# Performance work log

Measured on AMD Instinct MI355X. Metric: run time of the kernel, lower is better.

Reference implementation:

```python
import jax, jax.numpy as jnp
import numpy as np
from jax import lax

N = 100000   # total nodes in batched graph
E = 3200000  # total edges
B = 32       # graphs in batch
L = 1000     # text sequence length (required by mx3 kernel=108)
D = 128      # emb_dim
H = 3        # heads of gcn1
OD = 128     # output_dim


def setup_inputs() -> dict:
    key = jax.random.key(0)
    ks = jax.random.split(key, 32)
    def p(i, shape, s=0.05):
        return jax.random.normal(ks[i], shape, jnp.float32) * s
    return {
        "node_feat": p(0, (N, D), 1.0),
        "src": jax.random.randint(ks[1], (E,), 0, N),
        "dst": jax.random.randint(ks[2], (E,), 0, N),
        "graph_ids": jnp.sort(jax.random.randint(ks[3], (N,), 0, B)),
        "pad_dmap": p(4, (B, 1, L, D), 1.0),
        # GATConv 1: in=D, out=D, heads=3
        "W1": p(5, (D, H * D)), "al1": p(6, (H, D)), "ar1": p(7, (H, D)), "b1": p(8, (H * D,)),
        # GATConv 2: in=3D, out=3D, heads=1
        "W2": p(9, (H * D, H * D)), "al2": p(10, (1, H * D)), "ar2": p(11, (1, H * D)), "b2": p(12, (H * D,)),
        "fc_g1_w": p(13, (H * D, OD)), "fc_g1_b": p(14, (OD,)),
        # Conv1d weights in torch OIH layout
        "conv1_w": p(15, (128, D, 3)), "conv1_b": p(16, (128,)),
        "conv2_w": p(17, (128, 128, 3)), "conv2_b": p(18, (128,)),
        "conv3_w": p(19, (128, 128, 3)), "conv3_b": p(20, (128,)),
        "tf_w": p(21, (128, OD)), "tf_b": p(22, (OD,)),
        "w1": jnp.array([0.5], jnp.float32),
        "fc1_w": p(23, (OD, 512)), "fc1_b": p(24, (512,)),
        "fc2_w": p(25, (512, 256)), "fc2_b": p(26, (256,)),
        "out_w": p(27, (256, 2)), "out_b": p(28, (2,)),
    }


def _gat(feat, src, dst, W, al, ar, b, heads, od):
    """DGL GATConv (feat_drop=attn_drop=0, negative_slope=0.2, bias)."""
    n = feat.shape[0]
    h = (feat @ W).reshape(n, heads, od)                 # [N,H,od]
    el = jnp.einsum('nhd,hd->nh', h, al)                 # [N,H]
    er = jnp.einsum('nhd,hd->nh', h, ar)
    e = jax.nn.leaky_relu(el[src] + er[dst], 0.2)        # [E,H] per-edge score
    m = jax.ops.segment_max(e, dst, num_segments=n)
    m = jnp.where(jnp.isfinite(m), m, 0.0)               # isolated nodes -> 0
    a = jnp.exp(e - m[dst])
    s = jax.ops.segment_sum(a, dst, num_segments=n)
    alpha = a / s[dst]                                   # edge softmax over in-neighborhood
    rst = jax.ops.segment_sum(alpha[:, :, None] * h[src], dst, num_segments=n)
    return rst + b.reshape(1, heads, od)


def _conv1d(x, w, b):
    y = lax.conv_general_dilated(x, w, (1,), 'VALID', dimension_numbers=('NCH', 'OIH', 'NCH'))
    return y + b[None, :, None]


def _maxpool1d(x, k, s):
    return lax.reduce_window(x, -jnp.inf, lax.max, (1, 1, k), (1, 1, s), 'VALID')


def reference(node_feat, src, dst, graph_ids, pad_dmap,
              W1, al1, ar1, b1, W2, al2, ar2, b2,
              fc_g1_w, fc_g1_b, conv1_w, conv1_b, conv2_w, conv2_b,
              conv3_w, conv3_b, tf_w, tf_b, w1,
              fc1_w, fc1_b, fc2_w, fc2_b, out_w, out_b):
    relu = jax.nn.relu
    # graph branch
    g = relu(_gat(node_feat, src, dst, W1, al1, ar1, b1, H, D)).reshape(-1, H * D)
    g = relu(_gat(g, src, dst, W2, al2, ar2, b2, 1, H * D)).reshape(-1, H * D)
    gpool = jax.ops.segment_max(g, graph_ids, num_segments=B)   # graph max pooling [B,384]
    g1 = relu(gpool @ fc_g1_w + fc_g1_b)
    # text CNN branch
    x = pad_dmap[:, 0].transpose(0, 2, 1)                       # [B, D, L]
    f = _maxpool1d(_conv1d(x, conv1_w, conv1_b), 3, 3)
    f = _maxpool1d(_conv1d(f, conv2_w, conv2_b), 3, 3)
    f = _maxpool1d(_conv1d(f, conv3_w, conv3_b), 108, 1)[:, :, 0]  # [B,128]
    seq1 = relu(f @ tf_w + tf_b)
    # weighted fusion + MLP head (dropout is identity in eval)
    wv = jax.nn.sigmoid(w1)
    gc = (1.0 - wv) * g1 + wv * seq1
    gc = relu(gc @ fc1_w + fc1_b)
    gc = relu(gc @ fc2_w + fc2_b)
    o = relu(gc @ out_w + out_b)
    return jax.nn.softmax(o, axis=1)
```

## Files before the change

### kernel.cpp

```cpp
#include <hip/hip_runtime.h>
#include <math.h>

constexpr int NN = 100000;
constexpr int EE = 3200000;
constexpr int BB = 32;
constexpr int LSEQ = 1000;
constexpr int DD = 128;
constexpr int NH = 3;
constexpr int HD = 384;
constexpr int NB1 = (NN + 255) / 256;
constexpr int NMT = (NN + 127) / 128;

typedef __attribute__((ext_vector_type(8))) short bf16v8;
typedef __attribute__((ext_vector_type(4))) float f32x4;

static __device__ __forceinline__ float lrelu(float x) { return x > 0.f ? x : 0.2f * x; }
static __device__ __forceinline__ float bf2f(unsigned short u) {
  return __uint_as_float(((unsigned)u) << 16);
}
static __device__ __forceinline__ unsigned short f2bf(float f) {
  unsigned x = __float_as_uint(f);
  return (unsigned short)((x + 0x7fffu + ((x >> 16) & 1u)) >> 16);
}

constexpr int PB_NF   = (NN * DD / 4) / 256;
constexpr int PB_PAD  = (BB * LSEQ * 128 / 4) / 256;
constexpr int PB_DEG  = NB1;
constexpr int PB_EL2  = (2 * NN + 255) / 256;
constexpr int PB_GP   = (BB * HD + 255) / 256;
constexpr int PB_TW1  = (128 * 384 + 255) / 256;
constexpr int PB_TW2  = (384 * 384 + 255) / 256;
constexpr int PB_TC   = (128 * 384 + 255) / 256;
constexpr int PREP_BLOCKS = PB_NF + PB_PAD + PB_DEG + PB_EL2 + PB_GP + PB_TW1 + PB_TW2 + 3 * PB_TC;

__global__ void prep_misc(const float* __restrict__ nf, unsigned short* __restrict__ nfbf,
                          const float* __restrict__ pad, unsigned short* __restrict__ padbf,
                          int* __restrict__ deg, float* __restrict__ el2z,
                          unsigned* __restrict__ gpool,
                          const float* __restrict__ W1, unsigned short* __restrict__ Wt1,
                          const float* __restrict__ W2, unsigned short* __restrict__ Wt2,
                          const float* __restrict__ c1w, unsigned short* __restrict__ Wc1,
                          const float* __restrict__ c2w, unsigned short* __restrict__ Wc2,
                          const float* __restrict__ c3w, unsigned short* __restrict__ Wc3) {
  int bx = blockIdx.x, tid = threadIdx.x;
  if (bx < PB_NF) {
    int i = bx * 256 + tid;
    float4 v = ((const float4*)nf)[i];
    ushort4 o;
    o.x = f2bf(v.x); o.y = f2bf(v.y); o.z = f2bf(v.z); o.w = f2bf(v.w);
    ((ushort4*)nfbf)[i] = o;
    return;
  }
  bx -= PB_NF;
  if (bx < PB_PAD) {
    int i = bx * 256 + tid;
    float4 v = ((const float4*)pad)[i];
    ushort4 o;
    o.x = f2bf(v.x); o.y = f2bf(v.y); o.z = f2bf(v.z); o.w = f2bf(v.w);
    ((ushort4*)padbf)[i] = o;
    return;
  }
  bx -= PB_PAD;
  if (bx < PB_DEG) {
    int i = bx * 256 + tid;
    if (i < NN) deg[i] = 0;
    return;
  }
  bx -= PB_DEG;
  if (bx < PB_EL2) {
    int i = bx * 256 + tid;
    if (i < 2 * NN) el2z[i] = 0.f;
    return;
  }
  bx -= PB_EL2;
  if (bx < PB_GP) {
    int i = bx * 256 + tid;
    if (i < BB * HD) gpool[i] = 0u;
    return;
  }
  bx -= PB_GP;
  if (bx < PB_TW1) {
    int id = bx * 256 + tid;
    if (id < 384 * 128) { int n = id / 128, k = id % 128; Wt1[id] = f2bf(W1[(size_t)k * 384 + n]); }
    return;
  }
  bx -= PB_TW1;
  if (bx < PB_TW2) {
    int id = bx * 256 + tid;
    if (id < 384 * 384) { int n = id / 384, k = id % 384; Wt2[id] = f2bf(W2[(size_t)k * 384 + n]); }
    return;
  }
  bx -= PB_TW2;
  const float* cw = (bx < PB_TC) ? c1w : (bx < 2 * PB_TC) ? c2w : c3w;
  unsigned short* co = (bx < PB_TC) ? Wc1 : (bx < 2 * PB_TC) ? Wc2 : Wc3;
  int id = (bx % PB_TC) * 256 + tid;
  if (id < 128 * 384) {
    int o = id / 384, rem = id % 384;
    int t = rem / 128, i = rem % 128;
    co[id] = f2bf(cw[(size_t)o * 384 + i * 3 + t]);
  }
}

__global__ void hist_k(const int* __restrict__ dst, int* __restrict__ deg,
                       int* __restrict__ rank) {
  int i = blockIdx.x * 256 + threadIdx.x;
  if (i >= EE / 4) return;
  int4 d = ((const int4*)dst)[i];
  int4 r;
  r.x = atomicAdd(&deg[d.x], 1);
  r.y = atomicAdd(&deg[d.y], 1);
  r.z = atomicAdd(&deg[d.z], 1);
  r.w = atomicAdd(&deg[d.w], 1);
  ((int4*)rank)[i] = r;
}

__global__ void scan1_k(const int* __restrict__ deg, int* __restrict__ excl,
                        int* __restrict__ bsum) {
  __shared__ int tmp[256];
  int tid = threadIdx.x;
  int i = blockIdx.x * 256 + tid;
  int v = (i < NN) ? deg[i] : 0;
  tmp[tid] = v;
  __syncthreads();
  for (int off = 1; off < 256; off <<= 1) {
    int t = (tid >= off) ? tmp[tid - off] : 0;
    __syncthreads();
    tmp[tid] += t;
    __syncthreads();
  }
  if (i < NN) excl[i] = tmp[tid] - v;
  if (tid == 255) bsum[blockIdx.x] = tmp[255];
}

__global__ void scan2p(int* __restrict__ bsum) {
  __shared__ int tmp[512];
  int tid = threadIdx.x;
  int v = (tid < NB1) ? bsum[tid] : 0;
  tmp[tid] = v;
  __syncthreads();
  for (int off = 1; off < 512; off <<= 1) {
    int t = (tid >= off) ? tmp[tid - off] : 0;
    __syncthreads();
    tmp[tid] += t;
    __syncthreads();
  }
  if (tid < NB1) bsum[tid] = tmp[tid] - v;
}

__global__ void scan3_k(const int* __restrict__ excl, const int* __restrict__ bsum,
                        int* __restrict__ offs) {
  int i = blockIdx.x * 256 + threadIdx.x;
  if (i < NN) offs[i] = excl[i] + bsum[blockIdx.x];
}

__global__ void scatter_k(const int* __restrict__ src, const int* __restrict__ dst,
                          const int* __restrict__ rank, const int* __restrict__ offs,
                          int* __restrict__ srcs) {
  int i = blockIdx.x * 256 + threadIdx.x;
  if (i >= EE / 4) return;
  int4 s = ((const int4*)src)[i];
  int4 d = ((const int4*)dst)[i];
  int4 r = ((const int4*)rank)[i];
  srcs[offs[d.x] + r.x] = s.x;
  srcs[offs[d.y] + r.y] = s.y;
  srcs[offs[d.z] + r.z] = s.z;
  srcs[offs[d.w] + r.w] = s.w;
}

template <int NKB, bool BRES>
__global__ __launch_bounds__(512) void gemm_nres(const unsigned short* __restrict__ A,
                                                 const unsigned short* __restrict__ Bt,
                                                 unsigned short* __restrict__ C,
                                                 const float* __restrict__ al,
                                                 const float* __restrict__ ar,
                                                 float* __restrict__ el,
                                                 float* __restrict__ er,
                                                 int M, int Nc, int nmt, int mpb) {
  static_assert(!BRES || NKB <= 2, "resident B needs K<=128");
  constexpr int KTOT = NKB * 64;
  __shared__ unsigned short As[2][8192];
  __shared__ unsigned short Bs[16384];
  __shared__ float elbuf[128][4];
  __shared__ float erbuf[128][4];
  int tid = threadIdx.x;
  int lane = tid & 63;
  int wave = tid >> 6;
  int wm = wave >> 2, wn = wave & 3;
  int tile_n = blockIdx.x * 128;
  int rloc = lane >> 3;
  int cs = (lane & 7) ^ rloc;
  const unsigned short* Bb = Bt + (size_t)tile_n * KTOT;

  int c0 = tile_n + wn * 32 + (lane & 15);
  float alv0 = al[c0], alv1 = al[c0 + 16];
  float arv0 = ar[c0], arv1 = ar[c0 + 16];

  int mt0 = blockIdx.y * mpb;
  if (mt0 >= nmt) return;
  int mt1 = min(mt0 + mpb, nmt);

  auto stage_a = [&](int mt, int kb, int buf) {
    const unsigned short* Ab = A + (size_t)mt * 128 * KTOT;
    int mr = M - 1 - mt * 128;
#pragma unroll
    for (int q = 0; q < 2; ++q) {
      int t = wave * 2 + q, r = t * 8 + rloc;
      int ra = r > mr ? mr : r;
      __builtin_amdgcn_global_load_lds(
          (const __attribute__((address_space(1))) void*)(Ab + (size_t)ra * KTOT + kb * 64 + cs * 8),
          (__attribute__((address_space(3))) void*)(&As[buf][t * 512]), 16, 0, 0);
    }
  };
  auto stage_b = [&](int kb, int buf) {
#pragma unroll
    for (int q = 0; q < 2; ++q) {
      int t = wave * 2 + q, r = t * 8 + rloc;
      __builtin_amdgcn_global_load_lds(
          (const __attribute__((address_space(1))) void*)(Bb + (size_t)r * KTOT + kb * 64 + cs * 8),
          (__attribute__((address_space(3))) void*)(&Bs[buf * 8192 + t * 512]), 16, 0, 0);
    }
  };

  f32x4 acc[4][2];
#pragma unroll
  for (int i = 0; i < 4; ++i)
#pragma unroll
    for (int j = 0; j < 2; ++j) acc[i][j] = (f32x4){0.f, 0.f, 0.f, 0.f};

  if constexpr (BRES) {
#pragma unroll
    for (int kb = 0; kb < NKB; ++kb) stage_b(kb, kb);
  } else {
    stage_b(0, 0);
  }
  stage_a(mt0, 0, 0);
  __syncthreads();

  int nsteps = (mt1 - mt0) * NKB;
  for (int i = 0; i < nsteps; ++i) {
    int mt = mt0 + i / NKB;
    int kb = i % NKB;
    int cb = i & 1;
    if (i + 1 < nsteps) {
      int ni = i + 1;
      stage_a(mt0 + ni / NKB, ni % NKB, ni & 1);
      if constexpr (!BRES) stage_b(ni % NKB, ni & 1);
    }
    const unsigned short* Ablk = &As[cb][0];
    const unsigned short* Bblk = BRES ? (Bs + kb * 8192) : (Bs + cb * 8192);
#pragma unroll
    for (int ks = 0; ks < 2; ++ks) {
      int q = ks * 4 + (lane >> 4);
      bf16v8 af[4], bfr[2];
#pragma unroll
      for (int ii = 0; ii < 4; ++ii) {
        int r = wm * 64 + ii * 16 + (lane & 15);
        af[ii] = *(const bf16v8*)&Ablk[r * 64 + ((q ^ (r & 7)) * 8)];
      }
#pragma unroll
      for (int j = 0; j < 2; ++j) {
        int r = wn * 32 + j * 16 + (lane & 15);
        bfr[j] = *(const bf16v8*)&Bblk[r * 64 + ((q ^ (r & 7)) * 8)];
      }
#pragma unroll
      for (int ii = 0; ii < 4; ++ii)
#pragma unroll
        for (int j = 0; j < 2; ++j)
          acc[ii][j] = __builtin_amdgcn_mfma_f32_16x16x32_bf16(af[ii], bfr[j], acc[ii][j], 0, 0, 0);
    }
    if (kb == NKB - 1) {
#pragma unroll
      for (int ii = 0; ii < 4; ++ii) {
        int row0 = mt * 128 + wm * 64 + ii * 16 + (lane >> 4) * 4;
#pragma unroll
        for (int j = 0; j < 2; ++j) {
          int col = tile_n + wn * 32 + j * 16 + (lane & 15);
#pragma unroll
          for (int p = 0; p < 4; ++p) {
            int row = row0 + p;
            if (row < M) C[(size_t)row * Nc + col] = f2bf(acc[ii][j][p]);
          }
        }
      }
#pragma unroll
      for (int ii = 0; ii < 4; ++ii) {
#pragma unroll
        for (int p = 0; p < 4; ++p) {
          float pe = acc[ii][0][p] * alv0 + acc[ii][1][p] * alv1;
          float pr = acc[ii][0][p] * arv0 + acc[ii][1][p] * arv1;
#pragma unroll
          for (int off = 1; off < 16; off <<= 1) {
            pe += __shfl_xor(pe, off);
            pr += __shfl_xor(pr, off);
          }
          if ((lane & 15) == 0) {
            int rl = wm * 64 + ii * 16 + (lane >> 4) * 4 + p;
            elbuf[rl][wn] = pe;
            erbuf[rl][wn] = pr;
          }
        }
      }
      __syncthreads();
      if (tid < 128) {
        int row = mt * 128 + tid;
        if (row < M) {
          float ev = elbuf[tid][0] + elbuf[tid][1] + elbuf[tid][2] + elbuf[tid][3];
          float rv = erbuf[tid][0] + erbuf[tid][1] + erbuf[tid][2] + erbuf[tid][3];
          if constexpr (BRES) {
            el[row * 4 + blockIdx.x] = ev;
            er[row * 4 + blockIdx.x] = rv;
          } else {
            atomicAdd(&el[row], ev);
            atomicAdd(&er[row], rv);
          }
        }
      }
#pragma unroll
      for (int ii = 0; ii < 4; ++ii)
#pragma unroll
        for (int j = 0; j < 2; ++j) acc[ii][j] = (f32x4){0.f, 0.f, 0.f, 0.f};
    }
    __syncthreads();
  }
}

__global__ __launch_bounds__(256) void gemm_mfma(const unsigned short* __restrict__ A,
                                                 int lda,
                                                 const unsigned short* __restrict__ Bt,
                                                 unsigned short* __restrict__ C,
                                                 int M, int K, int Nc,
                                                 const float* __restrict__ bias,
                                                 long aBatch, long cBatch) {
  __shared__ unsigned short As[128 * 64];
  __shared__ unsigned short Bs[128 * 64];
  int lane = threadIdx.x & 63;
  int wave = threadIdx.x >> 6;
  int wm = wave >> 1, wn = wave & 1;
  int tile_m = blockIdx.y * 128;
  int tile_n = blockIdx.x * 128;
  int maxRa = M - 1 - tile_m;
  f32x4 acc[4][4];
#pragma unroll
  for (int i = 0; i < 4; ++i)
#pragma unroll
    for (int j = 0; j < 4; ++j) acc[i][j] = (f32x4){0.f, 0.f, 0.f, 0.f};

  const unsigned short* Ab = A + (size_t)blockIdx.z * aBatch + (size_t)tile_m * lda;
  unsigned short* Cb = C + (size_t)blockIdx.z * cBatch;
  const unsigned short* Bb = Bt + (size_t)tile_n * K;
  int rloc = (lane >> 3);
  int cs = (lane & 7) ^ rloc;

  for (int k0 = 0; k0 < K; k0 += 64) {
#pragma unroll
    for (int q = 0; q < 4; ++q) {
      int t = wave * 4 + q;
      int r = t * 8 + rloc;
      int ra = r > maxRa ? maxRa : r;
      __builtin_amdgcn_global_load_lds(
          (const __attribute__((address_space(1))) void*)(Ab + (size_t)ra * lda + k0 + cs * 8),
          (__attribute__((address_space(3))) void*)(As + t * 512), 16, 0, 0);
      __builtin_amdgcn_global_load_lds(
          (const __attribute__((address_space(1))) void*)(Bb + (size_t)r * K + k0 + cs * 8),
          (__attribute__((address_space(3))) void*)(Bs + t * 512), 16, 0, 0);
    }
    __syncthreads();
#pragma unroll
    for (int ks = 0; ks < 2; ++ks) {
      int q = ks * 4 + (lane >> 4);
      bf16v8 af[4], bfr[4];
#pragma unroll
      for (int i = 0; i < 4; ++i) {
        int r = wm * 64 + i * 16 + (lane & 15);
        af[i] = *(const bf16v8*)&As[r * 64 + ((q ^ (r & 7)) * 8)];
      }
#pragma unroll
      for (int j = 0; j < 4; ++j) {
        int r = wn * 64 + j * 16 + (lane & 15);
        bfr[j] = *(const bf16v8*)&Bs[r * 64 + ((q ^ (r & 7)) * 8)];
      }
#pragma unroll
      for (int i = 0; i < 4; ++i)
#pragma unroll
        for (int j = 0; j < 4; ++j)
          acc[i][j] = __builtin_amdgcn_mfma_f32_16x16x32_bf16(af[i], bfr[j], acc[i][j], 0, 0, 0);
    }
    __syncthreads();
  }
#pragma unroll
  for (int i = 0; i < 4; ++i) {
    int row0 = tile_m + wm * 64 + i * 16 + (lane >> 4) * 4;
#pragma unroll
    for (int j = 0; j < 4; ++j) {
      int col = tile_n + wn * 64 + j * 16 + (lane & 15);
      float bv = bias ? bias[col] : 0.f;
#pragma unroll
      for (int p = 0; p < 4; ++p) {
        int row = row0 + p;
        if (row < M) Cb[(size_t)row * Nc + col] = f2bf(acc[i][j][p] + bv);
      }
    }
  }
}

template <int H>
static __device__ __forceinline__ void agg_body3(const float4 t,
                                                 const unsigned short* __restrict__ hfeat,
                                                 int lane, float acc[6]) {
  int s2 = __float_as_int(t.w);
  const unsigned short* hrow = hfeat + (size_t)s2 * HD;
  uint2 va = *(const uint2*)(hrow + lane * 4);
  unsigned vb = *(const unsigned*)(hrow + 256 + lane * 2);
  float wa = (H == 3) ? ((lane < 32) ? t.x : t.y) : t.x;
  float wc = (H == 3) ? t.z : t.x;
  acc[0] += wa * bf2f((unsigned short)(va.x & 0xffffu));
  acc[1] += wa * bf2f((unsigned short)(va.x >> 16));
  acc[2] += wa * bf2f((unsigned short)(va.y & 0xffffu));
  acc[3] += wa * bf2f((unsigned short)(va.y >> 16));
  acc[4] += wc * bf2f((unsigned short)(vb & 0xffffu));
  acc[5] += wc * bf2f((unsigned short)(vb >> 16));
}

template <int H>
static __device__ __forceinline__ void load_sc(const float* __restrict__ el,
                                               int s, const float erd[H], float sc[H]) {
  if constexpr (H == 3) {
    float4 e = ((const float4*)el)[s];
    sc[0] = lrelu(e.x + erd[0]);
    sc[1] = lrelu(e.y + erd[1]);
    sc[2] = lrelu(e.z + erd[2]);
  } else {
    sc[0] = lrelu(el[s] + erd[0]);
  }
}

template <int H>
__global__ __launch_bounds__(256) void agg_csr3(const int* __restrict__ offs,
                                                const int* __restrict__ deg,
                                                const int* __restrict__ srcs,
                                                const float* __restrict__ el,
                                                const float* __restrict__ er,
                                                const unsigned short* __restrict__ hfeat,
                                                const float* __restrict__ bias,
                                                unsigned short* __restrict__ outg) {
  __shared__ float wb[4][64][4];
  int wave = threadIdx.x >> 6, lane = threadIdx.x & 63;
  int d = blockIdx.x * 4 + wave;
  int o0 = offs[d], dg = deg[d];
  float erd[H];
  if constexpr (H == 3) {
    float4 e = ((const float4*)er)[d];
    erd[0] = e.x; erd[1] = e.y; erd[2] = e.z;
  } else {
    erd[0] = er[d];
  }
  float acc[6] = {0.f, 0.f, 0.f, 0.f, 0.f, 0.f};
  float wsum[H];
#pragma unroll
  for (int h = 0; h < H; ++h) wsum[h] = 0.f;

  if (dg <= 64) {
    bool has = lane < dg;
    int s = has ? srcs[o0 + lane] : 0;
    float sc[H], mh[H];
    load_sc<H>(el, s, erd, sc);
#pragma unroll
    for (int h = 0; h < H; ++h) {
      if (!has) sc[h] = -1e30f;
      mh[h] = sc[h];
#pragma unroll
      for (int off = 1; off < 64; off <<= 1) mh[h] = fmaxf(mh[h], __shfl_xor(mh[h], off));
    }
    float w0 = 0.f, w1 = 0.f, w2 = 0.f;
    if (has) {
      w0 = __expf(sc[0] - mh[0]);
      if constexpr (H == 3) {
        w1 = __expf(sc[1] - mh[1]);
        w2 = __expf(sc[2] - mh[2]);
      }
    }
    wsum[0] = w0;
    if constexpr (H == 3) { wsum[1] = w1; wsum[2] = w2; }
    *(float4*)&wb[wave][lane][0] = make_float4(w0, w1, w2, __int_as_float(s));
#pragma unroll 16
    for (int j = 0; j < dg; ++j) {
      float4 t = *(const float4*)&wb[wave][j][0];
      agg_body3<H>(t, hfeat, lane, acc);
    }
  } else {
    float mh[H];
#pragma unroll
    for (int h = 0; h < H; ++h) mh[h] = -1e30f;
    for (int e = lane; e < dg; e += 64) {
      int s = srcs[o0 + e];
      float sc[H];
      load_sc<H>(el, s, erd, sc);
#pragma unroll
      for (int h = 0; h < H; ++h) mh[h] = fmaxf(mh[h], sc[h]);
    }
#pragma unroll
    for (int h = 0; h < H; ++h) {
#pragma unroll
      for (int off = 1; off < 64; off <<= 1) mh[h] = fmaxf(mh[h], __shfl_xor(mh[h], off));
    }
    int nch = (dg + 63) >> 6;
    for (int ch = 0; ch < nch; ++ch) {
      int e = ch * 64 + lane;
      bool has = e < dg;
      int s = has ? srcs[o0 + e] : 0;
      float sc[H];
      load_sc<H>(el, s, erd, sc);
      float w0 = 0.f, w1 = 0.f, w2 = 0.f;
      if (has) {
        w0 = __expf(sc[0] - mh[0]);
        if constexpr (H == 3) {
          w1 = __expf(sc[1] - mh[1]);
          w2 = __expf(sc[2] - mh[2]);
        }
      }
      wsum[0] += w0;
      if constexpr (H == 3) { wsum[1] += w1; wsum[2] += w2; }
      *(float4*)&wb[wave][lane][0] = make_float4(w0, w1, w2, __int_as_float(s));
      int cnt = min(64, dg - ch * 64);
#pragma unroll 16
      for (int j = 0; j < cnt; ++j) {
        float4 t = *(const float4*)&wb[wave][j][0];
        agg_body3<H>(t, hfeat, lane, acc);
      }
    }
  }
#pragma unroll
  for (int h = 0; h < H; ++h) {
#pragma unroll
    for (int off = 1; off < 64; off <<= 1) wsum[h] += __shfl_xor(wsum[h], off);
  }
  float swA = (H == 3) ? ((lane < 32) ? wsum[0] : wsum[1]) : wsum[0];
  float swC = (H == 3) ? wsum[H - 1] : wsum[0];
  float invA = (dg > 0) ? 1.f / swA : 0.f;
  float invC = (dg > 0) ? 1.f / swC : 0.f;
  unsigned short* orow = outg + (size_t)d * HD;
  int cA = lane * 4, cB = 256 + lane * 2;
  float r0 = fmaxf(acc[0] * invA + bias[cA + 0], 0.f);
  float r1 = fmaxf(acc[1] * invA + bias[cA + 1], 0.f);
  float r2 = fmaxf(acc[2] * invA + bias[cA + 2], 0.f);
  float r3 = fmaxf(acc[3] * invA + bias[cA + 3], 0.f);
  float r4 = fmaxf(acc[4] * invC + bias[cB + 0], 0.f);
  float r5 = fmaxf(acc[5] * invC + bias[cB + 1], 0.f);
  uint2 pa;
  pa.x = (unsigned)f2bf(r0) | ((unsigned)f2bf(r1) << 16);
  pa.y = (unsigned)f2bf(r2) | ((unsigned)f2bf(r3) << 16);
  *(uint2*)(orow + cA) = pa;
  *(unsigned*)(orow + cB) = (unsigned)f2bf(r4) | ((unsigned)f2bf(r5) << 16);
}

__global__ void graph_pool(const unsigned short* __restrict__ g, const int* __restrict__ gid,
                           unsigned* __restrict__ gp) {
  int c = threadIdx.x;
  int n0 = blockIdx.x * 64;
  int nend = min(n0 + 64, NN);
  int cur = gid[n0];
  float mx = 0.f;
  for (int n = n0; n < nend; ++n) {
    int gg = gid[n];
    if (gg != cur) {
      atomicMax(&gp[cur * HD + c], __float_as_uint(mx));
      cur = gg; mx = 0.f;
    }
    mx = fmaxf(mx, bf2f(g[(size_t)n * HD + c]));
  }
  atomicMax(&gp[cur * HD + c], __float_as_uint(mx));
}

__global__ void maxpool_nhc(const unsigned short* __restrict__ in, unsigned short* __restrict__ out,
                            int Lin, int Lout, int total) {
  int idx = blockIdx.x * 256 + threadIdx.x;
  if (idx >= total) return;
  int c = idx & 127;
  int j = (idx >> 7) % Lout;
  int b = idx / (128 * Lout);
  const unsigned short* p = in + ((size_t)b * Lin + j * 3) * 128 + c;
  float m = bf2f(p[0]);
  m = fmaxf(m, bf2f(p[128]));
  m = fmaxf(m, bf2f(p[256]));
  out[idx] = f2bf(m);
}

__global__ void gpool_c3(const unsigned short* __restrict__ in, float* __restrict__ fvec) {
  int idx = blockIdx.x * 256 + threadIdx.x;
  if (idx >= BB * 128) return;
  int c = idx & 127, b = idx >> 7;
  const unsigned short* p = in + (size_t)b * 108 * 128 + c;
  float m = bf2f(p[0]);
  for (int t = 1; t < 108; ++t) m = fmaxf(m, bf2f(p[t * 128]));
  fvec[idx] = m;
}

__global__ __launch_bounds__(256) void head_all(const unsigned* __restrict__ gpool,
                                                const float* __restrict__ fvec,
                                                const float* __restrict__ fcgw,
                                                const float* __restrict__ fcgb,
                                                const float* __restrict__ tfw,
                                                const float* __restrict__ tfb,
                                                const float* __restrict__ w1s,
                                                const float* __restrict__ fc1w,
                                                const float* __restrict__ fc1b,
                                                const float* __restrict__ fc2w,
                                                const float* __restrict__ fc2b,
                                                const float* __restrict__ outw,
                                                const float* __restrict__ outb,
                                                float* __restrict__ out) {
  __shared__ float gl[HD];
  __shared__ float gcv[128];
  __shared__ float gc1[512];
  __shared__ float gc2[256];
  int b = blockIdx.x, tid = threadIdx.x;
  for (int c = tid; c < HD; c += 256) gl[c] = __uint_as_float(gpool[b * HD + c]);
  __syncthreads();
  float wv = 1.f / (1.f + __expf(-w1s[0]));
  if (tid < 128) {
    float a = fcgb[tid];
    for (int k = 0; k < HD; ++k) a += gl[k] * fcgw[(size_t)k * 128 + tid];
    float g1 = fmaxf(a, 0.f);
    float s = tfb[tid];
    const float* fv = fvec + b * 128;
    for (int k = 0; k < 128; ++k) s += fv[k] * tfw[(size_t)k * 128 + tid];
    float s1 = fmaxf(s, 0.f);
    gcv[tid] = (1.f - wv) * g1 + wv * s1;
  }
  __syncthreads();
#pragma unroll
  for (int q = 0; q < 2; ++q) {
    int j = tid + q * 256;
    float a = fc1b[j];
    for (int k = 0; k < 128; ++k) a += gcv[k] * fc1w[(size_t)k * 512 + j];
    gc1[j] = fmaxf(a, 0.f);
  }
  __syncthreads();
  {
    float a = fc2b[tid];
    for (int k = 0; k < 512; ++k) a += gc1[k] * fc2w[(size_t)k * 256 + tid];
    gc2[tid] = fmaxf(a, 0.f);
  }
  __syncthreads();
  if (tid < 64) {
    float p0 = 0.f, p1 = 0.f;
#pragma unroll
    for (int q = 0; q < 4; ++q) {
      float v = gc2[tid + q * 64];
      p0 += v * outw[(tid + q * 64) * 2 + 0];
      p1 += v * outw[(tid + q * 64) * 2 + 1];
    }
#pragma unroll
    for (int off = 32; off; off >>= 1) {
      p0 += __shfl_down(p0, off);
      p1 += __shfl_down(p1, off);
    }
    if (tid == 0) {
      float o0 = fmaxf(p0 + outb[0], 0.f), o1 = fmaxf(p1 + outb[1], 0.f);
      float mm = fmaxf(o0, o1);
      float e0 = __expf(o0 - mm), e1 = __expf(o1 - mm);
      float inv = 1.f / (e0 + e1);
      out[b * 2 + 0] = e0 * inv;
      out[b * 2 + 1] = e1 * inv;
    }
  }
}

extern "C" void kernel_launch(void* const* d_in, const int* in_sizes, int n_in,
                              void* d_out, int out_size, void* d_ws, size_t ws_size,
                              hipStream_t stream) {
  const float* node_feat = (const float*)d_in[0];
  const int*   src  = (const int*)d_in[1];
  const int*   dst  = (const int*)d_in[2];
  const int*   gids = (const int*)d_in[3];
  const float* pad  = (const float*)d_in[4];
  const float* W1   = (const float*)d_in[5];
  const float* al1  = (const float*)d_in[6];
  const float* ar1  = (const float*)d_in[7];
  const float* b1   = (const float*)d_in[8];
  const float* W2   = (const float*)d_in[9];
  const float* al2  = (const float*)d_in[10];
  const float* ar2  = (const float*)d_in[11];
  const float* b2   = (const float*)d_in[12];
  const float* fcgw = (const float*)d_in[13];
  const float* fcgb = (const float*)d_in[14];
  const float* c1w  = (const float*)d_in[15];
  const float* c1b  = (const float*)d_in[16];
  const float* c2w  = (const float*)d_in[17];
  const float* c2b  = (const float*)d_in[18];
  const float* c3w  = (const float*)d_in[19];
  const float* c3b  = (const float*)d_in[20];
  const float* tfw  = (const float*)d_in[21];
  const float* tfb  = (const float*)d_in[22];
  const float* w1s  = (const float*)d_in[23];
  const float* fc1w = (const float*)d_in[24];
  const float* fc1b = (const float*)d_in[25];
  const float* fc2w = (const float*)d_in[26];
  const float* fc2b = (const float*)d_in[27];
  const float* outw = (const float*)d_in[28];
  const float* outb = (const float*)d_in[29];
  float* out = (float*)d_out;
  char* base = (char*)d_ws;

  constexpr size_t SZ_BIG = (size_t)NN * HD * 2;
  unsigned short* hA = (unsigned short*)(base + 0);
  unsigned short* gB = (unsigned short*)(base + SZ_BIG);
  unsigned short* nfbf = gB;
  size_t o = 2 * SZ_BIG;
  unsigned short* Wt1 = (unsigned short*)(base + o); o += 384 * 128 * 2;
  unsigned short* Wt2 = (unsigned short*)(base + o); o += 384 * 384 * 2;
  unsigned short* Wc1 = (unsigned short*)(base + o); o += 128 * 384 * 2;
  unsigned short* Wc2 = (unsigned short*)(base + o); o += 128 * 384 * 2;
  unsigned short* Wc3 = (unsigned short*)(base + o); o += 128 * 384 * 2;
  int* deg    = (int*)(base + o); o += (size_t)NN * 4;
  int* offs   = (int*)(base + o); o += (size_t)NN * 4;
  int* excl   = (int*)(base + o); o += (size_t)NN * 4;
  int* bsum   = (int*)(base + o); o += 2048;
  int* srcs   = (int*)(base + o); o += (size_t)EE * 4;
  int* rank   = (int*)(base + o); o += (size_t)EE * 4;
  float* el1  = (float*)(base + o); o += (size_t)NN * 4 * 4;
  float* er1  = (float*)(base + o); o += (size_t)NN * 4 * 4;
  float* el2  = (float*)(base + o); o += (size_t)NN * 4;
  float* er2  = (float*)(base + o); o += (size_t)NN * 4;
  unsigned* gpool = (unsigned*)(base + o); o += (size_t)BB * HD * 4;
  float* fvec = (float*)(base + o); o += BB * 128 * 4;

  unsigned short* padbf = (unsigned short*)base;
  unsigned short* c1bf  = padbf + (size_t)BB * LSEQ * 128;
  unsigned short* p1bf  = c1bf + (size_t)BB * 998 * 128;
  unsigned short* c2bf  = p1bf + (size_t)BB * 332 * 128;
  unsigned short* p2bf  = c2bf + (size_t)BB * 330 * 128;
  unsigned short* c3bf  = p2bf + (size_t)BB * 110 * 128;

  prep_misc<<<PREP_BLOCKS, 256, 0, stream>>>(node_feat, nfbf, pad, padbf, deg, el2, gpool,
                                             W1, Wt1, W2, Wt2, c1w, Wc1, c2w, Wc2, c3w, Wc3);

  gemm_mfma<<<dim3(1, 8, BB), 256, 0, stream>>>(padbf, 128, Wc1, c1bf, 998, 384, 128, c1b,
                                                (long)LSEQ * 128, (long)998 * 128);
  maxpool_nhc<<<(BB * 332 * 128 + 255) / 256, 256, 0, stream>>>(c1bf, p1bf, 998, 332, BB * 332 * 128);
  gemm_mfma<<<dim3(1, 3, BB), 256, 0, stream>>>(p1bf, 128, Wc2, c2bf, 330, 384, 128, c2b,
                                                (long)332 * 128, (long)330 * 128);
  maxpool_nhc<<<(BB * 110 * 128 + 255) / 256, 256, 0, stream>>>(c2bf, p2bf, 330, 110, BB * 110 * 128);
  gemm_mfma<<<dim3(1, 1, BB), 256, 0, stream>>>(p2bf, 128, Wc3, c3bf, 108, 384, 128, c3b,
                                                (long)110 * 128, (long)108 * 128);
  gpool_c3<<<(BB * 128 + 255) / 256, 256, 0, stream>>>(c3bf, fvec);

  hist_k<<<EE / 1024, 256, 0, stream>>>(dst, deg, rank);
  scan1_k<<<NB1, 256, 0, stream>>>(deg, excl, bsum);
  scan2p<<<1, 512, 0, stream>>>(bsum);
  scan3_k<<<NB1, 256, 0, stream>>>(excl, bsum, offs);
  scatter_k<<<EE / 1024, 256, 0, stream>>>(src, dst, rank, offs, srcs);

  gemm_nres<2, true><<<dim3(3, (NMT + 9) / 10), 512, 0, stream>>>(
      nfbf, Wt1, hA, al1, ar1, el1, er1, NN, HD, NMT, 10);
  agg_csr3<3><<<NN / 4, 256, 0, stream>>>(offs, deg, srcs, el1, er1, hA, b1, gB);

  gemm_nres<6, false><<<dim3(3, (NMT + 9) / 10), 512, 0, stream>>>(
      gB, Wt2, hA, al2, ar2, el2, er2, NN, HD, NMT, 10);
  agg_csr3<1><<<NN / 4, 256, 0, stream>>>(offs, deg, srcs, el2, er2, hA, b2, gB);

  graph_pool<<<(NN + 63) / 64, 384, 0, stream>>>(gB, gids, gpool);
  head_all<<<BB, 256, 0, stream>>>(gpool, fvec, fcgw, fcgb, tfw, tfb, w1s,
                                   fc1w, fc1b, fc2w, fc2b, outw, outb, out);
}
```

Before: 1.264 ms.

## Fuse graph max-pooling into second GAT aggregation and text pool into head

The second aggregation kernel now does graph max-pooling itself with per-element atomicMax into the pooled buffer, instead of writing node features and running a separate pool kernel. Each lane now handles six contiguous channels, loaded with a uint3 access. The text-branch global max-pool kernel is folded into the head kernel. The aim is to avoid the full node-feature write and re-read plus two launches, but it adds millions of contended atomics on a few addresses.

```diff
diff --git a/kernel.cpp b/kernel.cpp
--- a/kernel.cpp
+++ b/kernel.cpp
@@ -406,19 +406,25 @@
 template <int H>
 static __device__ __forceinline__ void agg_body3(const float4 t,
                                                  const unsigned short* __restrict__ hfeat,
-                                                 int lane, float acc[6]) {
+                                                 int cbase, float acc[6]) {
   int s2 = __float_as_int(t.w);
-  const unsigned short* hrow = hfeat + (size_t)s2 * HD;
-  uint2 va = *(const uint2*)(hrow + lane * 4);
-  unsigned vb = *(const unsigned*)(hrow + 256 + lane * 2);
-  float wa = (H == 3) ? ((lane < 32) ? t.x : t.y) : t.x;
-  float wc = (H == 3) ? t.z : t.x;
-  acc[0] += wa * bf2f((unsigned short)(va.x & 0xffffu));
-  acc[1] += wa * bf2f((unsigned short)(va.x >> 16));
-  acc[2] += wa * bf2f((unsigned short)(va.y & 0xffffu));
-  acc[3] += wa * bf2f((unsigned short)(va.y >> 16));
-  acc[4] += wc * bf2f((unsigned short)(vb & 0xffffu));
-  acc[5] += wc * bf2f((unsigned short)(vb >> 16));
+  const unsigned short* hrow = hfeat + (size_t)s2 * HD + cbase;
+  uint3 v = *(const uint3*)hrow;
+  unsigned vv0 = v.x, vv1 = v.y, vv2 = v.z;
+#pragma unroll
+  for (int k = 0; k < 3; ++k) {
+    unsigned vk = (k == 0) ? vv0 : (k == 1) ? vv1 : vv2;
+    float wlo, whi;
+    if constexpr (H == 3) {
+      int clo = cbase + 2 * k;
+      wlo = (clo < 128) ? t.x : (clo < 256) ? t.y : t.z;
+      whi = (clo + 1 < 128) ? t.x : (clo + 1 < 256) ? t.y : t.z;
+    } else {
+      wlo = t.x; whi = t.x;
+    }
+    acc[2 * k] += wlo * bf2f((unsigned short)(vk & 0xffffu));
+    acc[2 * k + 1] += whi * bf2f((unsigned short)(vk >> 16));
+  }
 }
 
 template <int H>
@@ -434,7 +440,7 @@
   }
 }
 
-template <int H>
+template <int H, bool POOL>
 __global__ __launch_bounds__(256) void agg_csr3(const int* __restrict__ offs,
                                                 const int* __restrict__ deg,
                                                 const int* __restrict__ srcs,
@@ -442,10 +448,13 @@
                                                 const float* __restrict__ er,
                                                 const unsigned short* __restrict__ hfeat,
                                                 const float* __restrict__ bias,
-                                                unsigned short* __restrict__ outg) {
+                                                unsigned short* __restrict__ outg,
+                                                const int* __restrict__ gids,
+                                                unsigned* __restrict__ gpool) {
   __shared__ float wb[4][64][4];
   int wave = threadIdx.x >> 6, lane = threadIdx.x & 63;
   int d = blockIdx.x * 4 + wave;
+  int cbase = lane * 6;
   int o0 = offs[d], dg = deg[d];
   float erd[H];
   if constexpr (H == 3) {
@@ -485,7 +494,7 @@
 #pragma unroll 16
     for (int j = 0; j < dg; ++j) {
       float4 t = *(const float4*)&wb[wave][j][0];
-      agg_body3<H>(t, hfeat, lane, acc);
+      agg_body3<H>(t, hfeat, cbase, acc);
     }
   } else {
     float mh[H];
@@ -525,7 +534,7 @@
 #pragma unroll 16
       for (int j = 0; j < cnt; ++j) {
         float4 t = *(const float4*)&wb[wave][j][0];
-        agg_body3<H>(t, hfeat, lane, acc);
+        agg_body3<H>(t, hfeat, cbase, acc);
       }
     }
   }
@@ -534,41 +543,39 @@
 #pragma unroll
     for (int off = 1; off < 64; off <<= 1) wsum[h] += __shfl_xor(wsum[h], off);
   }
-  float swA = (H == 3) ? ((lane < 32) ? wsum[0] : wsum[1]) : wsum[0];
-  float swC = (H == 3) ? wsum[H - 1] : wsum[0];
-  float invA = (dg > 0) ? 1.f / swA : 0.f;
-  float invC = (dg > 0) ? 1.f / swC : 0.f;
-  unsigned short* orow = outg + (size_t)d * HD;
-  int cA = lane * 4, cB = 256 + lane * 2;
-  float r0 = fmaxf(acc[0] * invA + bias[cA + 0], 0.f);
-  float r1 = fmaxf(acc[1] * invA + bias[cA + 1], 0.f);
-  float r2 = fmaxf(acc[2] * invA + bias[cA + 2], 0.f);
-  float r3 = fmaxf(acc[3] * invA + bias[cA + 3], 0.f);
-  float r4 = fmaxf(acc[4] * invC + bias[cB + 0], 0.f);
-  float r5 = fmaxf(acc[5] * invC + bias[cB + 1], 0.f);
-  uint2 pa;
-  pa.x = (unsigned)f2bf(r0) | ((unsigned)f2bf(r1) << 16);
-  pa.y = (unsigned)f2bf(r2) | ((unsigned)f2bf(r3) << 16);
-  *(uint2*)(orow + cA) = pa;
-  *(unsigned*)(orow + cB) = (unsigned)f2bf(r4) | ((unsigned)f2bf(r5) << 16);
-}
-
-__global__ void graph_pool(const unsigned short* __restrict__ g, const int* __restrict__ gid,
-                           unsigned* __restrict__ gp) {
-  int c = threadIdx.x;
-  int n0 = blockIdx.x * 64;
-  int nend = min(n0 + 64, NN);
-  int cur = gid[n0];
-  float mx = 0.f;
-  for (int n = n0; n < nend; ++n) {
-    int gg = gid[n];
-    if (gg != cur) {
-      atomicMax(&gp[cur * HD + c], __float_as_uint(mx));
-      cur = gg; mx = 0.f;
-    }
-    mx = fmaxf(mx, bf2f(g[(size_t)n * HD + c]));
-  }
-  atomicMax(&gp[cur * HD + c], __float_as_uint(mx));
+  float inv0, inv1, inv2;
+  if constexpr (H == 3) {
+    inv0 = (dg > 0) ? 1.f / wsum[0] : 0.f;
+    inv1 = (dg > 0) ? 1.f / wsum[1] : 0.f;
+    inv2 = (dg > 0) ? 1.f / wsum[2] : 0.f;
+  } else {
+    inv0 = inv1 = inv2 = (dg > 0) ? 1.f / wsum[0] : 0.f;
+  }
+  int gid = POOL ? gids[d] : 0;
+  unsigned short* orow = outg + (size_t)d * HD + cbase;
+  unsigned pk[3];
+#pragma unroll
+  for (int k = 0; k < 3; ++k) {
+    int clo = cbase + 2 * k, chi = clo + 1;
+    float ilo, ihi;
+    if constexpr (H == 3) {
+      ilo = (clo < 128) ? inv0 : (clo < 256) ? inv1 : inv2;
+      ihi = (chi < 128) ? inv0 : (chi < 256) ? inv1 : inv2;
+    } else {
+      ilo = inv0; ihi = inv0;
+    }
+    float rlo = fmaxf(acc[2 * k] * ilo + bias[clo], 0.f);
+    float rhi = fmaxf(acc[2 * k + 1] * ihi + bias[chi], 0.f);
+    pk[k] = (unsigned)f2bf(rlo) | ((unsigned)f2bf(rhi) << 16);
+    if constexpr (POOL) {
+      atomicMax(&gpool[gid * HD + clo], __float_as_uint(rlo));
+      atomicMax(&gpool[gid * HD + chi], __float_as_uint(rhi));
+    }
+  }
+  if constexpr (!POOL) {
+    uint3 uv; uv.x = pk[0]; uv.y = pk[1]; uv.z = pk[2];
+    *(uint3*)orow = uv;
+  }
 }
 
 __global__ void maxpool_nhc(const unsigned short* __restrict__ in, unsigned short* __restrict__ out,
@@ -585,18 +592,8 @@
   out[idx] = f2bf(m);
 }
 
-__global__ void gpool_c3(const unsigned short* __restrict__ in, float* __restrict__ fvec) {
-  int idx = blockIdx.x * 256 + threadIdx.x;
-  if (idx >= BB * 128) return;
-  int c = idx & 127, b = idx >> 7;
-  const unsigned short* p = in + (size_t)b * 108 * 128 + c;
-  float m = bf2f(p[0]);
-  for (int t = 1; t < 108; ++t) m = fmaxf(m, bf2f(p[t * 128]));
-  fvec[idx] = m;
-}
-
 __global__ __launch_bounds__(256) void head_all(const unsigned* __restrict__ gpool,
-                                                const float* __restrict__ fvec,
+                                                const unsigned short* __restrict__ c3bf,
                                                 const float* __restrict__ fcgw,
                                                 const float* __restrict__ fcgb,
                                                 const float* __restrict__ tfw,
@@ -610,11 +607,18 @@
                                                 const float* __restrict__ outb,
                                                 float* __restrict__ out) {
   __shared__ float gl[HD];
+  __shared__ float fvs[128];
   __shared__ float gcv[128];
   __shared__ float gc1[512];
   __shared__ float gc2[256];
   int b = blockIdx.x, tid = threadIdx.x;
   for (int c = tid; c < HD; c += 256) gl[c] = __uint_as_float(gpool[b * HD + c]);
+  if (tid < 128) {
+    const unsigned short* p = c3bf + (size_t)b * 108 * 128 + tid;
+    float m = bf2f(p[0]);
+    for (int t = 1; t < 108; ++t) m = fmaxf(m, bf2f(p[t * 128]));
+    fvs[tid] = m;
+  }
   __syncthreads();
   float wv = 1.f / (1.f + __expf(-w1s[0]));
   if (tid < 128) {
@@ -622,8 +626,7 @@
     for (int k = 0; k < HD; ++k) a += gl[k] * fcgw[(size_t)k * 128 + tid];
     float g1 = fmaxf(a, 0.f);
     float s = tfb[tid];
-    const float* fv = fvec + b * 128;
-    for (int k = 0; k < 128; ++k) s += fv[k] * tfw[(size_t)k * 128 + tid];
+    for (int k = 0; k < 128; ++k) s += fvs[k] * tfw[(size_t)k * 128 + tid];
     float s1 = fmaxf(s, 0.f);
     gcv[tid] = (1.f - wv) * g1 + wv * s1;
   }
@@ -703,8 +706,8 @@
   char* base = (char*)d_ws;
 
   constexpr size_t SZ_BIG = (size_t)NN * HD * 2;
-  unsigned short* hA = (unsigned short*)(base + 0);
-  unsigned short* gB = (unsigned short*)(base + SZ_BIG);
+  unsigned short* hA   = (unsigned short*)(base + 0);
+  unsigned short* gB   = (unsigned short*)(base + SZ_BIG);
   unsigned short* nfbf = gB;
   size_t o = 2 * SZ_BIG;
   unsigned short* Wt1 = (unsigned short*)(base + o); o += 384 * 128 * 2;
@@ -712,6 +715,7 @@
   unsigned short* Wc1 = (unsigned short*)(base + o); o += 128 * 384 * 2;
   unsigned short* Wc2 = (unsigned short*)(base + o); o += 128 * 384 * 2;
   unsigned short* Wc3 = (unsigned short*)(base + o); o += 128 * 384 * 2;
+  unsigned short* c3bf = (unsigned short*)(base + o); o += (size_t)BB * 108 * 128 * 2;
   int* deg    = (int*)(base + o); o += (size_t)NN * 4;
   int* offs   = (int*)(base + o); o += (size_t)NN * 4;
   int* excl   = (int*)(base + o); o += (size_t)NN * 4;
@@ -723,14 +727,12 @@
   float* el2  = (float*)(base + o); o += (size_t)NN * 4;
   float* er2  = (float*)(base + o); o += (size_t)NN * 4;
   unsigned* gpool = (unsigned*)(base + o); o += (size_t)BB * HD * 4;
-  float* fvec = (float*)(base + o); o += BB * 128 * 4;
 
   unsigned short* padbf = (unsigned short*)base;
   unsigned short* c1bf  = padbf + (size_t)BB * LSEQ * 128;
   unsigned short* p1bf  = c1bf + (size_t)BB * 998 * 128;
   unsigned short* c2bf  = p1bf + (size_t)BB * 332 * 128;
   unsigned short* p2bf  = c2bf + (size_t)BB * 330 * 128;
-  unsigned short* c3bf  = p2bf + (size_t)BB * 110 * 128;
 
   prep_misc<<<PREP_BLOCKS, 256, 0, stream>>>(node_feat, nfbf, pad, padbf, deg, el2, gpool,
                                              W1, Wt1, W2, Wt2, c1w, Wc1, c2w, Wc2, c3w, Wc3);
@@ -743,7 +745,6 @@
   maxpool_nhc<<<(BB * 110 * 128 + 255) / 256, 256, 0, stream>>>(c2bf, p2bf, 330, 110, BB * 110 * 128);
   gemm_mfma<<<dim3(1, 1, BB), 256, 0, stream>>>(p2bf, 128, Wc3, c3bf, 108, 384, 128, c3b,
                                                 (long)110 * 128, (long)108 * 128);
-  gpool_c3<<<(BB * 128 + 255) / 256, 256, 0, stream>>>(c3bf, fvec);
 
   hist_k<<<EE / 1024, 256, 0, stream>>>(dst, deg, rank);
   scan1_k<<<NB1, 256, 0, stream>>>(deg, excl, bsum);
@@ -753,13 +754,14 @@
 
   gemm_nres<2, true><<<dim3(3, (NMT + 9) / 10), 512, 0, stream>>>(
       nfbf, Wt1, hA, al1, ar1, el1, er1, NN, HD, NMT, 10);
-  agg_csr3<3><<<NN / 4, 256, 0, stream>>>(offs, deg, srcs, el1, er1, hA, b1, gB);
+  agg_csr3<3, false><<<NN / 4, 256, 0, stream>>>(offs, deg, srcs, el1, er1, hA, b1, gB,
+                                                 nullptr, nullptr);
 
   gemm_nres<6, false><<<dim3(3, (NMT + 9) / 10), 512, 0, stream>>>(
       gB, Wt2, hA, al2, ar2, el2, er2, NN, HD, NMT, 10);
-  agg_csr3<1><<<NN / 4, 256, 0, stream>>>(offs, deg, srcs, el2, er2, hA, b2, gB);
-
-  graph_pool<<<(NN + 63) / 64, 384, 0, stream>>>(gB, gids, gpool);
-  head_all<<<BB, 256, 0, stream>>>(gpool, fvec, fcgw, fcgb, tfw, tfb, w1s,
+  agg_csr3<1, true><<<NN / 4, 256, 0, stream>>>(offs, deg, srcs, el2, er2, hA, b2, gB,
+                                                gids, gpool);
+
+  head_all<<<BB, 256, 0, stream>>>(gpool, c3bf, fcgw, fcgb, tfw, tfb, w1s,
                                    fc1w, fc1b, fc2w, fc2b, outw, outb, out);
 }
```

New measurement: 3.476 ms. 2.75x slower.
